# Performance work log

Hardware: AMD Instinct MI355X
Metric: run time of the kernel (lower is better)

## Reference

```python
import jax, jax.numpy as jnp
import numpy as np

N_NODES = 100000
D = 128        # input_dim / feature dim
H = 128        # hidden_dim
O = 64         # output_dim (classes)
B = 4096       # batch of seed nodes
S = 16         # sample_num (neighbor fan-out)


def setup_inputs() -> dict:
    key = jax.random.key(0)
    k1, k2, k3, k4, k5, k6, k7 = jax.random.split(key, 7)
    nodes = jax.random.randint(k1, (B,), 0, N_NODES)
    neighbors_1 = jax.random.randint(k2, (B, S), 0, N_NODES)
    neighbors_2 = jax.random.randint(k3, (B * S, S), 0, N_NODES)
    node_features = jax.random.normal(k4, (N_NODES, D), dtype=jnp.float32)
    # xavier-uniform, no bias (matches nn.Linear weight layout [out, in])
    def xavier(k, out_d, in_d):
        lim = float(np.sqrt(6.0 / (in_d + out_d)))
        return jax.random.uniform(k, (out_d, in_d), jnp.float32, -lim, lim)
    W1 = xavier(k5, H, 2 * D)   # fc_layer_1 (concat=True -> input_dim*2)
    W2 = xavier(k6, H, 2 * D)   # fc_layer_2
    Wo = xavier(k7, O, H)       # output_layer
    return {"nodes": nodes, "neighbors_1": neighbors_1, "neighbors_2": neighbors_2,
            "node_features": node_features, "W1": W1, "W2": W2, "Wo": Wo}


def reference(nodes, neighbors_1, neighbors_2, node_features, W1, W2, Wo):
    # Level-1 neighbor node list (flattened samples of the seed nodes)
    neighs_nodes_1 = neighbors_1.reshape(-1)                 # [B*S]
    features_origin = node_features[nodes]                   # [B, D]
    features_1 = node_features[neighs_nodes_1]               # [B*S, D]

    # aggregator_1: mean over sampled 2-hop neighbors of each level-1 node
    agg_feat_1 = node_features[neighbors_2].mean(axis=1)     # [B*S, D]
    agg_feat_1 = jnp.concatenate([features_1, agg_feat_1], axis=-1)  # [B*S, 2D]
    agg_embed_1 = jax.nn.relu(agg_feat_1 @ W1.T)             # [B*S, H] (unused downstream, as in original)

    # aggregator_2: mean over sampled 1-hop neighbors of each seed node
    agg_feat_2 = node_features[neighbors_1].mean(axis=1)     # [B, D]
    agg_feat_2 = jnp.concatenate([features_origin, agg_feat_2], axis=-1)  # [B, 2D]
    agg_embed_2 = jax.nn.relu(agg_feat_2 @ W2.T)             # [B, H]

    logits = agg_embed_2 @ Wo.T                              # [B, O]
    return jax.nn.softmax(logits, axis=-1)
```

## Files before the change

kernel.cpp:

```cpp
#include <hip/hip_runtime.h>


constexpr int D = 128;
constexpr int H = 128;
constexpr int O = 64;
constexpr int S = 16;
constexpr int NB = 4096;
constexpr int SPB = 4;
constexpr int THREADS = 256;

__global__ __launch_bounds__(THREADS, 4) void sage_fused(
    const int* __restrict__ nodes,
    const int* __restrict__ neighbors_1,
    const float* __restrict__ node_features,
    const float* __restrict__ W2,
    const float* __restrict__ Wo,
    float* __restrict__ out)
{
    __shared__ float cat[SPB][2 * D];
    __shared__ float part[THREADS][9];
    __shared__ float h[SPB][H];

    const int t = threadIdx.x;
    const int seed0 = blockIdx.x * SPB;

    {
        const int lane = t & 63;
        const int r    = __builtin_amdgcn_readfirstlane(t >> 6);
        const int d4   = lane & 31;
        const int sub  = lane >> 5;
        const float4* nf = reinterpret_cast<const float4*>(node_features);

        const int4* nbp = reinterpret_cast<const int4*>(
            neighbors_1 + (size_t)(seed0 + r) * S + sub * 8);
        const int4 n0 = nbp[0];
        const int4 n1 = nbp[1];

        float4 sum = make_float4(0.f, 0.f, 0.f, 0.f);
        const int ids[8] = {n0.x, n0.y, n0.z, n0.w, n1.x, n1.y, n1.z, n1.w};
        #pragma unroll
        for (int s = 0; s < 8; ++s) {
            const float4 v = nf[(size_t)ids[s] * (D / 4) + d4];
            sum.x += v.x; sum.y += v.y; sum.z += v.z; sum.w += v.w;
        }
        float4 tot;
        tot.x = sum.x + __shfl_xor(sum.x, 32);
        tot.y = sum.y + __shfl_xor(sum.y, 32);
        tot.z = sum.z + __shfl_xor(sum.z, 32);
        tot.w = sum.w + __shfl_xor(sum.w, 32);

        if (sub == 0) {
            const int org = nodes[seed0 + r];
            const float4 ov = nf[(size_t)org * (D / 4) + d4];
            *reinterpret_cast<float4*>(&cat[r][4 * d4]) = ov;
        } else {
            const float4 mean = make_float4(tot.x * (1.f / 16.f), tot.y * (1.f / 16.f),
                                            tot.z * (1.f / 16.f), tot.w * (1.f / 16.f));
            *reinterpret_cast<float4*>(&cat[r][D + 4 * d4]) = mean;
        }
    }
    __syncthreads();

    {
        const int j0 = t & 63;
        const int q  = t >> 6;
        const float* w0 = W2 + (size_t)j0 * (2 * D) + q * 64;
        const float* w1 = W2 + (size_t)(j0 + 64) * (2 * D) + q * 64;
        float acc[SPB][2];
        #pragma unroll
        for (int r = 0; r < SPB; ++r) { acc[r][0] = 0.f; acc[r][1] = 0.f; }

        for (int k = 0; k < 64; k += 4) {
            const float4 a0 = *reinterpret_cast<const float4*>(w0 + k);
            const float4 a1 = *reinterpret_cast<const float4*>(w1 + k);
            #pragma unroll
            for (int r = 0; r < SPB; ++r) {
                const float4 c = *reinterpret_cast<const float4*>(&cat[r][q * 64 + k]);
                acc[r][0] = fmaf(a0.x, c.x, acc[r][0]);
                acc[r][0] = fmaf(a0.y, c.y, acc[r][0]);
                acc[r][0] = fmaf(a0.z, c.z, acc[r][0]);
                acc[r][0] = fmaf(a0.w, c.w, acc[r][0]);
                acc[r][1] = fmaf(a1.x, c.x, acc[r][1]);
                acc[r][1] = fmaf(a1.y, c.y, acc[r][1]);
                acc[r][1] = fmaf(a1.z, c.z, acc[r][1]);
                acc[r][1] = fmaf(a1.w, c.w, acc[r][1]);
            }
        }
        #pragma unroll
        for (int r = 0; r < SPB; ++r) {
            part[t][r * 2 + 0] = acc[r][0];
            part[t][r * 2 + 1] = acc[r][1];
        }
    }
    __syncthreads();

    for (int i = t; i < SPB * H; i += THREADS) {
        const int r  = i >> 7;
        const int j  = i & (H - 1);
        const int jj = j >> 6;
        const int j0 = j & 63;
        float v = 0.f;
        #pragma unroll
        for (int q = 0; q < 4; ++q) v += part[(q << 6) | j0][r * 2 + jj];
        h[r][j] = v > 0.f ? v : 0.f;
    }
    __syncthreads();

    {
        const int lane = t & 63;
        const int r    = t >> 6;
        const float* wo = Wo + (size_t)lane * H;
        float acc = 0.f;
        #pragma unroll
        for (int k = 0; k < H; k += 4) {
            const float4 wv = *reinterpret_cast<const float4*>(wo + k);
            acc = fmaf(wv.x, h[r][k + 0], acc);
            acc = fmaf(wv.y, h[r][k + 1], acc);
            acc = fmaf(wv.z, h[r][k + 2], acc);
            acc = fmaf(wv.w, h[r][k + 3], acc);
        }
        float m = acc;
        #pragma unroll
        for (int off = 32; off >= 1; off >>= 1)
            m = fmaxf(m, __shfl_xor(m, off));
        const float e = __expf(acc - m);
        float ssum = e;
        #pragma unroll
        for (int off = 32; off >= 1; off >>= 1)
            ssum += __shfl_xor(ssum, off);
        out[(size_t)(seed0 + r) * O + lane] = e / ssum;
    }
}

extern "C" void kernel_launch(void* const* d_in, const int* in_sizes, int n_in,
                              void* d_out, int out_size, void* d_ws, size_t ws_size,
                              hipStream_t stream) {
    const int*   nodes         = (const int*)d_in[0];
    const int*   neighbors_1   = (const int*)d_in[1];
    const float* node_features = (const float*)d_in[3];
    const float* W2            = (const float*)d_in[5];
    const float* Wo            = (const float*)d_in[6];
    float*       out           = (float*)d_out;

    sage_fused<<<NB / SPB, THREADS, 0, stream>>>(
        nodes, neighbors_1, node_features, W2, Wo, out);
}
```

Measured before the change: 138.4 us.

## Split gather and MLP into two kernels with LDS-staged swizzled weights

Splits the fused kernel in two. A one-wave-per-seed gather kernel writes the concatenated features to workspace, and a separate MLP kernel handles 8 seeds per block. The MLP kernel stages W2 in K-chunks through double-buffered, XOR-swizzled shared memory with register prefetch, and loads Wo into swizzled LDS, so the weights are reused across more seeds instead of being read from global per thread. The cost is an extra launch and a global round-trip of the intermediate concat buffer.

```diff
diff --git a/kernel.cpp b/kernel.cpp
--- a/kernel.cpp
+++ b/kernel.cpp
@@ -6,129 +6,163 @@
 constexpr int O = 64;
 constexpr int S = 16;
 constexpr int NB = 4096;
-constexpr int SPB = 4;
-constexpr int THREADS = 256;
 
-__global__ __launch_bounds__(THREADS, 4) void sage_fused(
+__global__ __launch_bounds__(64) void k_gather(
     const int* __restrict__ nodes,
-    const int* __restrict__ neighbors_1,
-    const float* __restrict__ node_features,
+    const int* __restrict__ neigh,
+    const float* __restrict__ nf,
+    float* __restrict__ cat)
+{
+    const int seed = blockIdx.x;
+    const int lane = threadIdx.x;
+    const int d4   = lane & 31;
+    const int sub  = lane >> 5;
+    const float4* nf4 = reinterpret_cast<const float4*>(nf);
+
+    const int4* nbp = reinterpret_cast<const int4*>(neigh + (size_t)seed * S + sub * 8);
+    const int4 n0 = nbp[0], n1 = nbp[1];
+    const int ids[8] = {n0.x, n0.y, n0.z, n0.w, n1.x, n1.y, n1.z, n1.w};
+
+    float4 sum = make_float4(0.f, 0.f, 0.f, 0.f);
+    #pragma unroll
+    for (int s = 0; s < 8; ++s) {
+        const float4 v = nf4[(size_t)ids[s] * (D / 4) + d4];
+        sum.x += v.x; sum.y += v.y; sum.z += v.z; sum.w += v.w;
+    }
+    float4 tot;
+    tot.x = sum.x + __shfl_xor(sum.x, 32);
+    tot.y = sum.y + __shfl_xor(sum.y, 32);
+    tot.z = sum.z + __shfl_xor(sum.z, 32);
+    tot.w = sum.w + __shfl_xor(sum.w, 32);
+
+    float4* o4 = reinterpret_cast<float4*>(cat + (size_t)seed * (2 * D));
+    if (sub == 0) {
+        o4[d4] = nf4[(size_t)nodes[seed] * (D / 4) + d4];
+    } else {
+        o4[32 + d4] = make_float4(tot.x * 0.0625f, tot.y * 0.0625f,
+                                  tot.z * 0.0625f, tot.w * 0.0625f);
+    }
+}
+
+constexpr int SPB = 8;
+constexpr int KP  = 32;
+
+__global__ __launch_bounds__(256, 2) void k_mlp(
+    const float* __restrict__ cat,
     const float* __restrict__ W2,
     const float* __restrict__ Wo,
     float* __restrict__ out)
 {
-    __shared__ float cat[SPB][2 * D];
-    __shared__ float part[THREADS][9];
-    __shared__ float h[SPB][H];
+    __shared__ float catl[SPB][2 * D];
+    __shared__ float w2l[2][H][KP];
+    __shared__ float wol[O][D];
+    __shared__ float hl[SPB][H];
 
-    const int t = threadIdx.x;
-    const int seed0 = blockIdx.x * SPB;
+    const int t  = threadIdx.x;
+    const int s0 = blockIdx.x * SPB;
+
+    float4 pv[4];
+    #pragma unroll
+    for (int i = 0; i < 4; ++i) {
+        const int idx = t + i * 256, row = idx >> 3, c4 = idx & 7;
+        pv[i] = *reinterpret_cast<const float4*>(W2 + (size_t)row * (2 * D) + c4 * 4);
+    }
+    float4 cv0, cv1;
+    {
+        const float4* cg = reinterpret_cast<const float4*>(cat + (size_t)s0 * 2 * D);
+        cv0 = cg[t]; cv1 = cg[t + 256];
+    }
+    float4 wv[8];
+    #pragma unroll
+    for (int i = 0; i < 8; ++i)
+        wv[i] = reinterpret_cast<const float4*>(Wo)[t + i * 256];
 
     {
-        const int lane = t & 63;
-        const int r    = __builtin_amdgcn_readfirstlane(t >> 6);
-        const int d4   = lane & 31;
-        const int sub  = lane >> 5;
-        const float4* nf = reinterpret_cast<const float4*>(node_features);
+        float4* cl = reinterpret_cast<float4*>(&catl[0][0]);
+        cl[t] = cv0; cl[t + 256] = cv1;
+    }
+    #pragma unroll
+    for (int i = 0; i < 8; ++i) {
+        const int idx = t + i * 256, c = idx >> 5, k4 = idx & 31;
+        *reinterpret_cast<float4*>(&wol[c][((k4 & 24) | ((k4 ^ c) & 7)) << 2]) = wv[i];
+    }
 
-        const int4* nbp = reinterpret_cast<const int4*>(
-            neighbors_1 + (size_t)(seed0 + r) * S + sub * 8);
-        const int4 n0 = nbp[0];
-        const int4 n1 = nbp[1];
+    const int j0 = t & 63;
+    const int sg = t >> 6;
+    const int sA = sg * 2, sB = sA + 1;
+    const int swz = j0 & 7;
+    float acc00 = 0.f, acc01 = 0.f, acc10 = 0.f, acc11 = 0.f;
 
-        float4 sum = make_float4(0.f, 0.f, 0.f, 0.f);
-        const int ids[8] = {n0.x, n0.y, n0.z, n0.w, n1.x, n1.y, n1.z, n1.w};
+    for (int p = 0; p < 8; ++p) {
+        const int cur = p & 1;
         #pragma unroll
-        for (int s = 0; s < 8; ++s) {
-            const float4 v = nf[(size_t)ids[s] * (D / 4) + d4];
-            sum.x += v.x; sum.y += v.y; sum.z += v.z; sum.w += v.w;
+        for (int i = 0; i < 4; ++i) {
+            const int idx = t + i * 256, row = idx >> 3, c4 = idx & 7;
+            *reinterpret_cast<float4*>(&w2l[cur][row][(c4 ^ (row & 7)) << 2]) = pv[i];
         }
-        float4 tot;
-        tot.x = sum.x + __shfl_xor(sum.x, 32);
-        tot.y = sum.y + __shfl_xor(sum.y, 32);
-        tot.z = sum.z + __shfl_xor(sum.z, 32);
-        tot.w = sum.w + __shfl_xor(sum.w, 32);
+        __syncthreads();
+        if (p < 7) {
+            #pragma unroll
+            for (int i = 0; i < 4; ++i) {
+                const int idx = t + i * 256, row = idx >> 3, c4 = idx & 7;
+                pv[i] = *reinterpret_cast<const float4*>(
+                    W2 + (size_t)row * (2 * D) + (p + 1) * KP + c4 * 4);
+            }
+        }
+        #pragma unroll
+        for (int k4 = 0; k4 < 8; ++k4) {
+            const float4 wA = *reinterpret_cast<const float4*>(&w2l[cur][j0][(k4 ^ swz) << 2]);
+            const float4 wB = *reinterpret_cast<const float4*>(&w2l[cur][j0 + 64][(k4 ^ swz) << 2]);
+            const float4 cA = *reinterpret_cast<const float4*>(&catl[sA][p * KP + k4 * 4]);
+            const float4 cB = *reinterpret_cast<const float4*>(&catl[sB][p * KP + k4 * 4]);
+            acc00 = fmaf(wA.x, cA.x, acc00); acc00 = fmaf(wA.y, cA.y, acc00);
+            acc00 = fmaf(wA.z, cA.z, acc00); acc00 = fmaf(wA.w, cA.w, acc00);
+            acc01 = fmaf(wA.x, cB.x, acc01); acc01 = fmaf(wA.y, cB.y, acc01);
+            acc01 = fmaf(wA.z, cB.z, acc01); acc01 = fmaf(wA.w, cB.w, acc01);
+            acc10 = fmaf(wB.x, cA.x, acc10); acc10 = fmaf(wB.y, cA.y, acc10);
+            acc10 = fmaf(wB.z, cA.z, acc10); acc10 = fmaf(wB.w, cA.w, acc10);
+            acc11 = fmaf(wB.x, cB.x, acc11); acc11 = fmaf(wB.y, cB.y, acc11);
+            acc11 = fmaf(wB.z, cB.z, acc11); acc11 = fmaf(wB.w, cB.w, acc11);
+        }
+        __syncthreads();
+    }
 
-        if (sub == 0) {
-            const int org = nodes[seed0 + r];
-            const float4 ov = nf[(size_t)org * (D / 4) + d4];
-            *reinterpret_cast<float4*>(&cat[r][4 * d4]) = ov;
-        } else {
-            const float4 mean = make_float4(tot.x * (1.f / 16.f), tot.y * (1.f / 16.f),
-                                            tot.z * (1.f / 16.f), tot.w * (1.f / 16.f));
-            *reinterpret_cast<float4*>(&cat[r][D + 4 * d4]) = mean;
-        }
-    }
+    hl[sA][j0]      = acc00 > 0.f ? acc00 : 0.f;
+    hl[sB][j0]      = acc01 > 0.f ? acc01 : 0.f;
+    hl[sA][j0 + 64] = acc10 > 0.f ? acc10 : 0.f;
+    hl[sB][j0 + 64] = acc11 > 0.f ? acc11 : 0.f;
     __syncthreads();
 
     {
-        const int j0 = t & 63;
-        const int q  = t >> 6;
-        const float* w0 = W2 + (size_t)j0 * (2 * D) + q * 64;
-        const float* w1 = W2 + (size_t)(j0 + 64) * (2 * D) + q * 64;
-        float acc[SPB][2];
+        const int c = t & 63;
+        const int cswz = c & 7;
+        float a0 = 0.f, a1 = 0.f;
         #pragma unroll
-        for (int r = 0; r < SPB; ++r) { acc[r][0] = 0.f; acc[r][1] = 0.f; }
-
-        for (int k = 0; k < 64; k += 4) {
-            const float4 a0 = *reinterpret_cast<const float4*>(w0 + k);
-            const float4 a1 = *reinterpret_cast<const float4*>(w1 + k);
-            #pragma unroll
-            for (int r = 0; r < SPB; ++r) {
-                const float4 c = *reinterpret_cast<const float4*>(&cat[r][q * 64 + k]);
-                acc[r][0] = fmaf(a0.x, c.x, acc[r][0]);
-                acc[r][0] = fmaf(a0.y, c.y, acc[r][0]);
-                acc[r][0] = fmaf(a0.z, c.z, acc[r][0]);
-                acc[r][0] = fmaf(a0.w, c.w, acc[r][0]);
-                acc[r][1] = fmaf(a1.x, c.x, acc[r][1]);
-                acc[r][1] = fmaf(a1.y, c.y, acc[r][1]);
-                acc[r][1] = fmaf(a1.z, c.z, acc[r][1]);
-                acc[r][1] = fmaf(a1.w, c.w, acc[r][1]);
-            }
+        for (int k4 = 0; k4 < 32; ++k4) {
+            const float4 w = *reinterpret_cast<const float4*>(
+                &wol[c][((k4 & 24) | ((k4 ^ cswz) & 7)) << 2]);
+            const float4 h0 = *reinterpret_cast<const float4*>(&hl[sA][k4 * 4]);
+            const float4 h1 = *reinterpret_cast<const float4*>(&hl[sB][k4 * 4]);
+            a0 = fmaf(w.x, h0.x, a0); a0 = fmaf(w.y, h0.y, a0);
+            a0 = fmaf(w.z, h0.z, a0); a0 = fmaf(w.w, h0.w, a0);
+            a1 = fmaf(w.x, h1.x, a1); a1 = fmaf(w.y, h1.y, a1);
+            a1 = fmaf(w.z, h1.z, a1); a1 = fmaf(w.w, h1.w, a1);
         }
+        float m0 = a0, m1 = a1;
         #pragma unroll
-        for (int r = 0; r < SPB; ++r) {
-            part[t][r * 2 + 0] = acc[r][0];
-            part[t][r * 2 + 1] = acc[r][1];
+        for (int off = 32; off >= 1; off >>= 1) {
+            m0 = fmaxf(m0, __shfl_xor(m0, off));
+            m1 = fmaxf(m1, __shfl_xor(m1, off));
         }
-    }
-    __syncthreads();
-
-    for (int i = t; i < SPB * H; i += THREADS) {
-        const int r  = i >> 7;
-        const int j  = i & (H - 1);
-        const int jj = j >> 6;
-        const int j0 = j & 63;
-        float v = 0.f;
+        const float e0 = __expf(a0 - m0), e1 = __expf(a1 - m1);
+        float z0 = e0, z1 = e1;
         #pragma unroll
-        for (int q = 0; q < 4; ++q) v += part[(q << 6) | j0][r * 2 + jj];
-        h[r][j] = v > 0.f ? v : 0.f;
-    }
-    __syncthreads();
-
-    {
-        const int lane = t & 63;
-        const int r    = t >> 6;
-        const float* wo = Wo + (size_t)lane * H;
-        float acc = 0.f;
-        #pragma unroll
-        for (int k = 0; k < H; k += 4) {
-            const float4 wv = *reinterpret_cast<const float4*>(wo + k);
-            acc = fmaf(wv.x, h[r][k + 0], acc);
-            acc = fmaf(wv.y, h[r][k + 1], acc);
-            acc = fmaf(wv.z, h[r][k + 2], acc);
-            acc = fmaf(wv.w, h[r][k + 3], acc);
+        for (int off = 32; off >= 1; off >>= 1) {
+            z0 += __shfl_xor(z0, off);
+            z1 += __shfl_xor(z1, off);
         }
-        float m = acc;
-        #pragma unroll
-        for (int off = 32; off >= 1; off >>= 1)
-            m = fmaxf(m, __shfl_xor(m, off));
-        const float e = __expf(acc - m);
-        float ssum = e;
-        #pragma unroll
-        for (int off = 32; off >= 1; off >>= 1)
-            ssum += __shfl_xor(ssum, off);
-        out[(size_t)(seed0 + r) * O + lane] = e / ssum;
+        out[(size_t)(s0 + sA) * O + c] = e0 / z0;
+        out[(size_t)(s0 + sB) * O + c] = e1 / z1;
     }
 }
 
@@ -141,7 +175,8 @@
     const float* W2            = (const float*)d_in[5];
     const float* Wo            = (const float*)d_in[6];
     float*       out           = (float*)d_out;
+    float*       cat           = (float*)d_ws;
 
-    sage_fused<<<NB / SPB, THREADS, 0, stream>>>(
-        nodes, neighbors_1, node_features, W2, Wo, out);
+    k_gather<<<NB, 64, 0, stream>>>(nodes, neighbors_1, node_features, cat);
+    k_mlp<<<NB / SPB, 256, 0, stream>>>(cat, W2, Wo, out);
 }
```

New measurement: 126.6 us. 8.5% less time.
